# Performance work log

Hardware: AMD Instinct MI355X
Metric: run time of the kernel (lower is better)

Reference implementation:

```python
import jax, jax.numpy as jnp
import numpy as np

JACCARD_THRESH = 0.5
NEGPOS_RATIO = 3
VAR = (0.1, 0.2)


def point_form(p):
    # center-size (cx,cy,w,h) -> corner (xmin,ymin,xmax,ymax)
    return jnp.concatenate([p[:, :2] - p[:, 2:] / 2, p[:, :2] + p[:, 2:] / 2], axis=1)


def jaccard(a, b):
    # a: [No,4] corner boxes, b: [Np,4] corner boxes -> IoU [No,Np]
    lt = jnp.maximum(a[:, None, :2], b[None, :, :2])
    rb = jnp.minimum(a[:, None, 2:], b[None, :, 2:])
    wh = jnp.clip(rb - lt, 0.0)
    inter = wh[..., 0] * wh[..., 1]
    area_a = ((a[:, 2] - a[:, 0]) * (a[:, 3] - a[:, 1]))[:, None]
    area_b = ((b[:, 2] - b[:, 0]) * (b[:, 3] - b[:, 1]))[None, :]
    return inter / (area_a + area_b - inter)


def encode(matched, priors):
    # matched: [Np,4] corner GT, priors: [Np,4] center-size
    g_cxcy = ((matched[:, :2] + matched[:, 2:]) / 2 - priors[:, :2]) / (VAR[0] * priors[:, 2:])
    g_wh = jnp.log((matched[:, 2:] - matched[:, :2]) / priors[:, 2:]) / VAR[1]
    return jnp.concatenate([g_cxcy, g_wh], axis=1)


def match_one(truths, labels, priors):
    # truths: [No,4], labels: [No], priors: [Np,4] center-size
    overlaps = jaccard(truths, point_form(priors))          # [No,Np]
    best_prior_idx = jnp.argmax(overlaps, axis=1)           # [No]
    best_truth_overlap = jnp.max(overlaps, axis=0)          # [Np]
    best_truth_idx = jnp.argmax(overlaps, axis=0)           # [Np]
    # each GT keeps its best prior (overlap forced to 2)
    best_truth_overlap = best_truth_overlap.at[best_prior_idx].set(2.0)
    best_truth_idx = best_truth_idx.at[best_prior_idx].set(jnp.arange(truths.shape[0]))
    matched = truths[best_truth_idx]                        # [Np,4]
    conf = labels[best_truth_idx].astype(jnp.int32) + 1     # background = 0
    conf = jnp.where(best_truth_overlap < JACCARD_THRESH, 0, conf)
    return encode(matched, priors), conf


def reference(loc_data, conf_data, dbox_list, targets):
    num_batch, num_dbox, num_classes = conf_data.shape
    truths = targets[:, :, :4]
    labels = targets[:, :, 4]
    loc_t, conf_t = jax.vmap(match_one, in_axes=(0, 0, None))(truths, labels, dbox_list)
    pos_mask = conf_t > 0                                   # [B,Np]
    # localization loss: SmoothL1 (beta=1), summed over positive dboxes
    diff = loc_data - loc_t
    ad = jnp.abs(diff)
    sl1 = jnp.where(ad < 1.0, 0.5 * diff * diff, ad - 0.5)
    loss_l = jnp.sum(sl1 * pos_mask[..., None].astype(sl1.dtype))
    # per-dbox cross entropy
    logp = jax.nn.log_softmax(conf_data, axis=-1)
    ce = -jnp.take_along_axis(logp, conf_t[..., None], axis=-1)[..., 0]  # [B,Np]
    # hard negative mining: rank (descending) of pos-zeroed CE via double argsort
    loss_c_hnm = jnp.where(pos_mask, 0.0, ce)
    loss_idx = jnp.argsort(-loss_c_hnm, axis=1)
    idx_rank = jnp.argsort(loss_idx, axis=1)
    num_pos = jnp.sum(pos_mask, axis=1, keepdims=True)      # [B,1]
    num_neg = jnp.minimum(num_pos * NEGPOS_RATIO, num_dbox)
    neg_mask = idx_rank < num_neg
    sel = jnp.logical_or(pos_mask, neg_mask)
    loss_c = jnp.sum(jnp.where(sel, ce, 0.0))
    N = jnp.sum(num_pos).astype(loss_l.dtype)
    return loss_l / N, loss_c / N


def setup_inputs() -> dict:
    key = jax.random.key(0)
    ks = jax.random.split(key, 7)
    B, Np, C, No = 128, 8732, 21, 16
    loc_data = jax.random.normal(ks[0], (B, Np, 4), dtype=jnp.float32) * 0.1
    conf_data = jax.random.normal(ks[1], (B, Np, C), dtype=jnp.float32)
    # default boxes in center-size form, w/h strictly positive
    cxcy = jax.random.uniform(ks[2], (Np, 2), minval=0.05, maxval=0.95)
    wh = jax.random.uniform(ks[3], (Np, 2), minval=0.05, maxval=0.5)
    dbox_list = jnp.concatenate([cxcy, wh], axis=1).astype(jnp.float32)
    # ground truth: valid corner-form boxes + class label in [0,20)
    gcxcy = jax.random.uniform(ks[4], (B, No, 2), minval=0.2, maxval=0.8)
    gwh = jax.random.uniform(ks[5], (B, No, 2), minval=0.05, maxval=0.3)
    boxes = jnp.concatenate([gcxcy - gwh / 2, gcxcy + gwh / 2], axis=-1)
    lab = jax.random.randint(ks[6], (B, No, 1), 0, C - 1).astype(jnp.float32)
    targets = jnp.concatenate([boxes, lab], axis=-1).astype(jnp.float32)
    return {"loc_data": loc_data, "conf_data": conf_data, "dbox_list": dbox_list, "targets": targets}
```

## Files before the change

kernel.cpp:

```cpp
#include <hip/hip_runtime.h>
#include <stdint.h>

#define TPB 256
#define PPT 2
#define SELTPB 1024
#define SELWAVES (SELTPB / 64)
#define MAXNO 64
#define NMB 16

__device__ __forceinline__ float sl1f(float d) {
    float ad = fabsf(d);
    return ad < 1.0f ? 0.5f * d * d : ad - 0.5f;
}

__device__ __forceinline__ float iou_pair(float tx1, float ty1, float tx2, float ty2, float ta,
                                          float px1, float py1, float px2, float py2, float pa) {
    float ltx = fmaxf(tx1, px1), lty = fmaxf(ty1, py1);
    float rbx = fminf(tx2, px2), rby = fminf(ty2, py2);
    float wx = fmaxf(rbx - ltx, 0.0f), wy = fmaxf(rby - lty, 0.0f);
    float inter = wx * wy;
    return inter / ((ta + pa) - inter);
}

template <int NO>
__global__ __launch_bounds__(256) void match_partial_kernel(
    const float* __restrict__ dbox, const float* __restrict__ targets,
    unsigned long long* __restrict__ pkeys, unsigned* __restrict__ done, int Np, int No) {
    int b = blockIdx.y, mb = blockIdx.x;
    int tid = threadIdx.x;
    if (mb == 0 && b == 0 && tid == 0) *done = 0u;
    __shared__ float s_t[NO][5];
    __shared__ unsigned long long s_k[4][NO];
    if (tid < No) {
        const float* tr = targets + ((size_t)b * No + tid) * 5;
        float x1 = tr[0], y1 = tr[1], x2 = tr[2], y2 = tr[3];
        s_t[tid][0] = x1; s_t[tid][1] = y1; s_t[tid][2] = x2; s_t[tid][3] = y2;
        s_t[tid][4] = (x2 - x1) * (y2 - y1);
    }
    __syncthreads();
    int clen = (Np + NMB - 1) / NMB;
    int start = mb * clen;
    int end = start + clen;
    if (end > Np) end = Np;
    unsigned long long key[NO];
#pragma unroll
    for (int t = 0; t < NO; ++t) key[t] = 0ull;
    for (int p = start + tid; p < end; p += 256) {
        float4 pr = *reinterpret_cast<const float4*>(dbox + (size_t)p * 4);
        float px1 = pr.x - pr.z * 0.5f, py1 = pr.y - pr.w * 0.5f;
        float px2 = pr.x + pr.z * 0.5f, py2 = pr.y + pr.w * 0.5f;
        float pa = (px2 - px1) * (py2 - py1);
        unsigned lowp = 0xFFFFFFFFu - (unsigned)p;
#pragma unroll
        for (int t = 0; t < NO; ++t) {
            float iou = iou_pair(s_t[t][0], s_t[t][1], s_t[t][2], s_t[t][3], s_t[t][4],
                                 px1, py1, px2, py2, pa);
            unsigned long long k =
                (((unsigned long long)__float_as_uint(iou)) << 32) | (unsigned long long)lowp;
            if (k > key[t]) key[t] = k;
        }
    }
    int lane = tid & 63, wv = tid >> 6;
#pragma unroll
    for (int t = 0; t < NO; ++t) {
        unsigned long long k = key[t];
        for (int off = 32; off; off >>= 1) {
            unsigned long long o = __shfl_down(k, off);
            if (o > k) k = o;
        }
        if (lane == 0) s_k[wv][t] = k;
    }
    __syncthreads();
    if (tid < No) {
        unsigned long long m = s_k[0][tid];
#pragma unroll
        for (int w = 1; w < 4; ++w)
            if (s_k[w][tid] > m) m = s_k[w][tid];
        pkeys[((size_t)b * NMB + mb) * No + tid] = m;
    }
}

template <int CC, int TNO>
__global__ __launch_bounds__(TPB, 1) void main_kernel(
    const float* __restrict__ loc, const float* __restrict__ conf,
    const float* __restrict__ dbox, const float* __restrict__ targets,
    const unsigned long long* __restrict__ pkeys,
    float* __restrict__ v, float* __restrict__ part_l, float* __restrict__ part_c,
    int* __restrict__ part_n, int Np, int C, int No, int nchunk) {
    __shared__ float s_tb[(TNO > 0 ? TNO : MAXNO)][6];
    __shared__ unsigned s_ovr[(TNO > 0 ? TNO : MAXNO)];
    __shared__ float s_red1[4];
    __shared__ float s_red2[4];
    __shared__ int s_redi[4];
    int b = blockIdx.y, chunk = blockIdx.x, tid = threadIdx.x;
    int pbase = chunk * (TPB * PPT);
    if (tid < No) {
        const float* tr = targets + ((size_t)b * No + tid) * 5;
        float x1 = tr[0], y1 = tr[1], x2 = tr[2], y2 = tr[3];
        s_tb[tid][0] = x1; s_tb[tid][1] = y1; s_tb[tid][2] = x2; s_tb[tid][3] = y2;
        s_tb[tid][4] = (x2 - x1) * (y2 - y1);
        s_tb[tid][5] = tr[4];
        unsigned long long k = pkeys[((size_t)b * NMB + 0) * No + tid];
#pragma unroll
        for (int m = 1; m < NMB; ++m) {
            unsigned long long kk = pkeys[((size_t)b * NMB + m) * No + tid];
            if (kk > k) k = kk;
        }
        s_ovr[tid] = 0xFFFFFFFFu - (unsigned)(k & 0xFFFFFFFFull);
    }
    __syncthreads();

    float px1[PPT], py1[PPT], px2[PPT], py2[PPT], pa[PPT];
    float bov[PPT];
    int bidx[PPT], ovt[PPT];
    bool vld[PPT];
#pragma unroll
    for (int pp = 0; pp < PPT; ++pp) {
        int p = pbase + pp * TPB + tid;
        vld[pp] = p < Np;
        bov[pp] = -1.0f; bidx[pp] = 0; ovt[pp] = -1;
        if (vld[pp]) {
            float4 pr = *reinterpret_cast<const float4*>(dbox + (size_t)p * 4);
            px1[pp] = pr.x - pr.z * 0.5f; py1[pp] = pr.y - pr.w * 0.5f;
            px2[pp] = pr.x + pr.z * 0.5f; py2[pp] = pr.y + pr.w * 0.5f;
            pa[pp] = (px2[pp] - px1[pp]) * (py2[pp] - py1[pp]);
        } else {
            px1[pp] = 0; py1[pp] = 0; px2[pp] = 0; py2[pp] = 0; pa[pp] = 0;
        }
    }
    int nt = (TNO > 0) ? TNO : No;
    for (int t = 0; t < nt; ++t) {
        float tx1 = s_tb[t][0], ty1 = s_tb[t][1], tx2 = s_tb[t][2], ty2 = s_tb[t][3];
        float ta = s_tb[t][4];
        unsigned ov = s_ovr[t];
#pragma unroll
        for (int pp = 0; pp < PPT; ++pp) {
            int p = pbase + pp * TPB + tid;
            float iou = iou_pair(tx1, ty1, tx2, ty2, ta,
                                 px1[pp], py1[pp], px2[pp], py2[pp], pa[pp]);
            if (iou > bov[pp]) { bov[pp] = iou; bidx[pp] = t; }
            if (ov == (unsigned)p) ovt[pp] = t;
        }
    }

    float lossl = 0.0f, posce = 0.0f;
    int npos = 0;
#pragma unroll
    for (int pp = 0; pp < PPT; ++pp) {
        if (!vld[pp]) continue;
        int p = pbase + pp * TPB + tid;
        int bi = bidx[pp];
        float bv = bov[pp];
        if (ovt[pp] >= 0) { bi = ovt[pp]; bv = 2.0f; }
        int ct = (bv < 0.5f) ? 0 : ((int)s_tb[bi][5] + 1);
        const float* crow = conf + ((size_t)b * Np + p) * C;
        float ce;
        if (CC == 21) {
            float4 q0 = *reinterpret_cast<const float4*>(crow + 0);
            float4 q1 = *reinterpret_cast<const float4*>(crow + 4);
            float4 q2 = *reinterpret_cast<const float4*>(crow + 8);
            float4 q3 = *reinterpret_cast<const float4*>(crow + 12);
            float4 q4 = *reinterpret_cast<const float4*>(crow + 16);
            float x20 = crow[20];
            float fc = q0.x;
            fc = (ct == 1) ? q0.y : fc;  fc = (ct == 2) ? q0.z : fc;
            fc = (ct == 3) ? q0.w : fc;  fc = (ct == 4) ? q1.x : fc;
            fc = (ct == 5) ? q1.y : fc;  fc = (ct == 6) ? q1.z : fc;
            fc = (ct == 7) ? q1.w : fc;  fc = (ct == 8) ? q2.x : fc;
            fc = (ct == 9) ? q2.y : fc;  fc = (ct == 10) ? q2.z : fc;
            fc = (ct == 11) ? q2.w : fc; fc = (ct == 12) ? q3.x : fc;
            fc = (ct == 13) ? q3.y : fc; fc = (ct == 14) ? q3.z : fc;
            fc = (ct == 15) ? q3.w : fc; fc = (ct == 16) ? q4.x : fc;
            fc = (ct == 17) ? q4.y : fc; fc = (ct == 18) ? q4.z : fc;
            fc = (ct == 19) ? q4.w : fc; fc = (ct == 20) ? x20 : fc;
            float s0 = __expf(q0.x) + __expf(q0.y) + __expf(q0.z) + __expf(q0.w);
            float s1 = __expf(q1.x) + __expf(q1.y) + __expf(q1.z) + __expf(q1.w);
            float s2 = __expf(q2.x) + __expf(q2.y) + __expf(q2.z) + __expf(q2.w);
            float s3 = __expf(q3.x) + __expf(q3.y) + __expf(q3.z) + __expf(q3.w);
            float s4 = __expf(q4.x) + __expf(q4.y) + __expf(q4.z) + __expf(q4.w);
            ce = __logf(((s0 + s1) + (s2 + s3)) + (s4 + __expf(x20))) - fc;
        } else {
            float mx = crow[0];
            for (int j = 1; j < C; ++j) mx = fmaxf(mx, crow[j]);
            float s = 0.0f;
            for (int j = 0; j < C; ++j) s += __expf(crow[j] - mx);
            ce = __logf(s) + mx - crow[ct];
        }
        bool pos = ct > 0;
        v[(size_t)b * Np + p] = pos ? 0.0f : ce;
        if (pos) {
            posce += ce;
            npos += 1;
            float mx1 = s_tb[bi][0], my1 = s_tb[bi][1];
            float mx2 = s_tb[bi][2], my2 = s_tb[bi][3];
            float pcx = (px1[pp] + px2[pp]) * 0.5f, pcy = (py1[pp] + py2[pp]) * 0.5f;
            float pw = px2[pp] - px1[pp], ph = py2[pp] - py1[pp];
            float gcx = ((mx1 + mx2) * 0.5f - pcx) / (0.1f * pw);
            float gcy = ((my1 + my2) * 0.5f - pcy) / (0.1f * ph);
            float gw = __logf((mx2 - mx1) / pw) / 0.2f;
            float gh = __logf((my2 - my1) / ph) / 0.2f;
            float4 l4 = *reinterpret_cast<const float4*>(loc + ((size_t)b * Np + p) * 4);
            lossl += sl1f(l4.x - gcx) + sl1f(l4.y - gcy) + sl1f(l4.z - gw) + sl1f(l4.w - gh);
        }
    }
    float a1 = lossl, a2 = posce;
    int ni = npos;
    for (int off = 32; off; off >>= 1) {
        a1 += __shfl_down(a1, off);
        a2 += __shfl_down(a2, off);
        ni += __shfl_down(ni, off);
    }
    if ((tid & 63) == 0) {
        s_red1[tid >> 6] = a1;
        s_red2[tid >> 6] = a2;
        s_redi[tid >> 6] = ni;
    }
    __syncthreads();
    if (tid == 0) {
        part_l[(size_t)b * nchunk + chunk] = s_red1[0] + s_red1[1] + s_red1[2] + s_red1[3];
        part_c[(size_t)b * nchunk + chunk] = s_red2[0] + s_red2[1] + s_red2[2] + s_red2[3];
        part_n[(size_t)b * nchunk + chunk] = s_redi[0] + s_redi[1] + s_redi[2] + s_redi[3];
    }
}

__global__ __launch_bounds__(SELTPB) void select_kernel(
    const float* __restrict__ v, const float* __restrict__ pl,
    const float* __restrict__ pc, const int* __restrict__ pn,
    float* __restrict__ row_res, unsigned* __restrict__ done,
    float* __restrict__ out, int Np, int nchunk, int negpos) {
    int b = blockIdx.x, tid = threadIdx.x;
    int lane = tid & 63, wv = tid >> 6;
    extern __shared__ unsigned sv[];
    __shared__ unsigned whist[SELWAVES][256];
    __shared__ float s_f[SELWAVES];
    __shared__ int s_dig, s_acc;
    __shared__ float s_lossl, s_posce;
    __shared__ int s_np;
    __shared__ int s_last;

    if (wv == 0) {
        float a = 0.0f, c = 0.0f;
        int n = 0;
        for (int i = lane; i < nchunk; i += 64) {
            a += pl[(size_t)b * nchunk + i];
            c += pc[(size_t)b * nchunk + i];
            n += pn[(size_t)b * nchunk + i];
        }
        for (int off = 32; off; off >>= 1) {
            a += __shfl_down(a, off);
            c += __shfl_down(c, off);
            n += __shfl_down(n, off);
        }
        if (lane == 0) { s_lossl = a; s_posce = c; s_np = n; }
    }
    {
        const float4* v4 = reinterpret_cast<const float4*>(v + (size_t)b * Np);
        int n4 = Np >> 2;
        for (int i = tid; i < n4; i += SELTPB) {
            float4 f = v4[i];
            uint4 u;
            u.x = __float_as_uint(f.x); u.y = __float_as_uint(f.y);
            u.z = __float_as_uint(f.z); u.w = __float_as_uint(f.w);
            *reinterpret_cast<uint4*>(&sv[i << 2]) = u;
        }
        for (int i = (n4 << 2) + tid; i < Np; i += SELTPB)
            sv[i] = __float_as_uint(v[(size_t)b * Np + i]);
    }
    __syncthreads();
    int npos = s_np;
    int K = npos * negpos;
    if (K > Np) K = Np;
    float lossc = s_posce;
    if (K > 0) {
        unsigned prefix = 0;
        int Krem = K;
        for (int shift = 24; shift >= 0; shift -= 8) {
            for (int i = tid; i < SELWAVES * 256; i += SELTPB)
                (&whist[0][0])[i] = 0;
            __syncthreads();
            for (int i = tid; i < Np; i += SELTPB) {
                unsigned u = sv[i];
                bool match = (shift == 24) || ((u >> (shift + 8)) == (prefix >> (shift + 8)));
                if (match) atomicAdd(&whist[wv][(u >> shift) & 0xFFu], 1u);
            }
            __syncthreads();
            if (wv == 0) {
                unsigned t0 = 0, t1 = 0, t2 = 0, t3 = 0;
#pragma unroll
                for (int w = 0; w < SELWAVES; ++w) {
                    t0 += whist[w][4 * lane + 0];
                    t1 += whist[w][4 * lane + 1];
                    t2 += whist[w][4 * lane + 2];
                    t3 += whist[w][4 * lane + 3];
                }
                unsigned s = t0 + t1 + t2 + t3;
                unsigned run = s;
                for (int off = 1; off < 64; off <<= 1) {
                    unsigned o = __shfl_down(run, off);
                    if (lane + off < 64) run += o;
                }
                unsigned hi = run - s;
                unsigned S3 = hi + t3, S2 = S3 + t2, S1 = S2 + t1, S0 = S1 + t0;
                unsigned kr = (unsigned)Krem;
                if (S3 >= kr && hi < kr) { s_dig = 4 * lane + 3; s_acc = (int)hi; }
                else if (S2 >= kr && S3 < kr) { s_dig = 4 * lane + 2; s_acc = (int)S3; }
                else if (S1 >= kr && S2 < kr) { s_dig = 4 * lane + 1; s_acc = (int)S2; }
                else if (S0 >= kr && S1 < kr) { s_dig = 4 * lane + 0; s_acc = (int)S1; }
            }
            __syncthreads();
            prefix |= ((unsigned)s_dig) << shift;
            Krem -= s_acc;
        }
        float sum_gt = 0.0f;
        for (int i = tid; i < Np; i += SELTPB) {
            unsigned u = sv[i];
            if (u > prefix) sum_gt += __uint_as_float(u);
        }
        for (int off = 32; off; off >>= 1) sum_gt += __shfl_down(sum_gt, off);
        if (lane == 0) s_f[wv] = sum_gt;
        __syncthreads();
        if (tid == 0) {
            float t = 0.0f;
            for (int w = 0; w < SELWAVES; ++w) t += s_f[w];
            lossc += t + (float)Krem * __uint_as_float(prefix);
        }
    }
    if (tid == 0) {
        row_res[(size_t)b * 3 + 0] = s_lossl;
        row_res[(size_t)b * 3 + 1] = lossc;
        row_res[(size_t)b * 3 + 2] = (float)npos;
        __threadfence();
        unsigned old = atomicAdd(done, 1u);
        s_last = (old == gridDim.x - 1) ? 1 : 0;
    }
    __syncthreads();
    if (s_last && wv == 0) {
        __threadfence();
        const volatile float* rr = (const volatile float*)row_res;
        float l = 0.0f, c = 0.0f, n = 0.0f;
        int B = (int)gridDim.x;
        for (int i = lane; i < B; i += 64) {
            l += rr[(size_t)i * 3 + 0];
            c += rr[(size_t)i * 3 + 1];
            n += rr[(size_t)i * 3 + 2];
        }
        for (int off = 32; off; off >>= 1) {
            l += __shfl_down(l, off);
            c += __shfl_down(c, off);
            n += __shfl_down(n, off);
        }
        if (lane == 0) {
            out[0] = l / n;
            out[1] = c / n;
        }
    }
}

extern "C" void kernel_launch(void* const* d_in, const int* in_sizes, int n_in,
                              void* d_out, int out_size, void* d_ws, size_t ws_size,
                              hipStream_t stream) {
    const float* loc = (const float*)d_in[0];
    const float* conf = (const float*)d_in[1];
    const float* dbox = (const float*)d_in[2];
    const float* targets = (const float*)d_in[3];

    int Np = in_sizes[2] / 4;
    int B = in_sizes[0] / (Np * 4);
    int C = in_sizes[1] / (B * Np);
    int No = in_sizes[3] / (B * 5);
    int nchunk = (Np + TPB * PPT - 1) / (TPB * PPT);

    char* w = (char*)d_ws;
    unsigned long long* pkeys = (unsigned long long*)w;
    w += (size_t)B * NMB * No * sizeof(unsigned long long);
    float* v = (float*)w;
    w += (size_t)B * Np * sizeof(float);
    float* part_l = (float*)w;
    w += (size_t)B * nchunk * sizeof(float);
    float* part_c = (float*)w;
    w += (size_t)B * nchunk * sizeof(float);
    int* part_n = (int*)w;
    w += (size_t)B * nchunk * sizeof(int);
    float* row_res = (float*)w;
    w += (size_t)B * 3 * sizeof(float);
    unsigned* done = (unsigned*)w;

    dim3 mgrid(NMB, B);
    if (No == 16)
        match_partial_kernel<16><<<mgrid, 256, 0, stream>>>(dbox, targets, pkeys, done, Np, No);
    else
        match_partial_kernel<MAXNO><<<mgrid, 256, 0, stream>>>(dbox, targets, pkeys, done, Np, No);

    dim3 grid(nchunk, B);
    if (C == 21 && No == 16)
        main_kernel<21, 16><<<grid, TPB, 0, stream>>>(loc, conf, dbox, targets, pkeys,
                                                      v, part_l, part_c, part_n, Np, C, No, nchunk);
    else
        main_kernel<0, 0><<<grid, TPB, 0, stream>>>(loc, conf, dbox, targets, pkeys,
                                                    v, part_l, part_c, part_n, Np, C, No, nchunk);
    select_kernel<<<B, SELTPB, (size_t)Np * sizeof(float), stream>>>(
        v, part_l, part_c, part_n, row_res, done, (float*)d_out, Np, nchunk, 3);
}
```

Baseline: 79.15 us.

## Hoist conf log-sum-exp before IoU matching, double points per thread

Moves the 21-class log-sum-exp computation ahead of the prior/GT IoU loop, so the large conf loads are issued early and can overlap with the matching arithmetic. The target logit is then fetched with one scalar load instead of a select chain. PPT rises from 2 to 4 and launch bounds now target 2 blocks per CU, giving fewer blocks with more work each. The general-C fallback path is removed, so the code now assumes C == 21 with no max subtraction, and register pressure grows from holding four rows' state.

```diff
diff --git a/kernel.cpp b/kernel.cpp
--- a/kernel.cpp
+++ b/kernel.cpp
@@ -2,7 +2,7 @@
 #include <stdint.h>
 
 #define TPB 256
-#define PPT 2
+#define PPT 4
 #define SELTPB 1024
 #define SELWAVES (SELTPB / 64)
 #define MAXNO 64
@@ -81,7 +81,7 @@
 }
 
 template <int CC, int TNO>
-__global__ __launch_bounds__(TPB, 1) void main_kernel(
+__global__ __launch_bounds__(TPB, 2) void main_kernel(
     const float* __restrict__ loc, const float* __restrict__ conf,
     const float* __restrict__ dbox, const float* __restrict__ targets,
     const unsigned long long* __restrict__ pkeys,
@@ -110,16 +110,36 @@
     }
     __syncthreads();
 
+    float lse[PPT];
+#pragma unroll
+    for (int pp = 0; pp < PPT; ++pp) {
+        int p = pbase + pp * TPB + tid;
+        lse[pp] = 0.0f;
+        if (p < Np) {
+            const float* crow = conf + ((size_t)b * Np + p) * (CC > 0 ? CC : 21);
+            float4 q0 = *reinterpret_cast<const float4*>(crow + 0);
+            float4 q1 = *reinterpret_cast<const float4*>(crow + 4);
+            float4 q2 = *reinterpret_cast<const float4*>(crow + 8);
+            float4 q3 = *reinterpret_cast<const float4*>(crow + 12);
+            float4 q4 = *reinterpret_cast<const float4*>(crow + 16);
+            float x20 = crow[20];
+            float s0 = __expf(q0.x) + __expf(q0.y) + __expf(q0.z) + __expf(q0.w);
+            float s1 = __expf(q1.x) + __expf(q1.y) + __expf(q1.z) + __expf(q1.w);
+            float s2 = __expf(q2.x) + __expf(q2.y) + __expf(q2.z) + __expf(q2.w);
+            float s3 = __expf(q3.x) + __expf(q3.y) + __expf(q3.z) + __expf(q3.w);
+            float s4 = __expf(q4.x) + __expf(q4.y) + __expf(q4.z) + __expf(q4.w);
+            lse[pp] = __logf(((s0 + s1) + (s2 + s3)) + (s4 + __expf(x20)));
+        }
+    }
+
     float px1[PPT], py1[PPT], px2[PPT], py2[PPT], pa[PPT];
     float bov[PPT];
     int bidx[PPT], ovt[PPT];
-    bool vld[PPT];
 #pragma unroll
     for (int pp = 0; pp < PPT; ++pp) {
         int p = pbase + pp * TPB + tid;
-        vld[pp] = p < Np;
         bov[pp] = -1.0f; bidx[pp] = 0; ovt[pp] = -1;
-        if (vld[pp]) {
+        if (p < Np) {
             float4 pr = *reinterpret_cast<const float4*>(dbox + (size_t)p * 4);
             px1[pp] = pr.x - pr.z * 0.5f; py1[pp] = pr.y - pr.w * 0.5f;
             px2[pp] = pr.x + pr.z * 0.5f; py2[pp] = pr.y + pr.w * 0.5f;
@@ -147,45 +167,14 @@
     int npos = 0;
 #pragma unroll
     for (int pp = 0; pp < PPT; ++pp) {
-        if (!vld[pp]) continue;
         int p = pbase + pp * TPB + tid;
+        if (p >= Np) continue;
         int bi = bidx[pp];
         float bv = bov[pp];
         if (ovt[pp] >= 0) { bi = ovt[pp]; bv = 2.0f; }
         int ct = (bv < 0.5f) ? 0 : ((int)s_tb[bi][5] + 1);
-        const float* crow = conf + ((size_t)b * Np + p) * C;
-        float ce;
-        if (CC == 21) {
-            float4 q0 = *reinterpret_cast<const float4*>(crow + 0);
-            float4 q1 = *reinterpret_cast<const float4*>(crow + 4);
-            float4 q2 = *reinterpret_cast<const float4*>(crow + 8);
-            float4 q3 = *reinterpret_cast<const float4*>(crow + 12);
-            float4 q4 = *reinterpret_cast<const float4*>(crow + 16);
-            float x20 = crow[20];
-            float fc = q0.x;
-            fc = (ct == 1) ? q0.y : fc;  fc = (ct == 2) ? q0.z : fc;
-            fc = (ct == 3) ? q0.w : fc;  fc = (ct == 4) ? q1.x : fc;
-            fc = (ct == 5) ? q1.y : fc;  fc = (ct == 6) ? q1.z : fc;
-            fc = (ct == 7) ? q1.w : fc;  fc = (ct == 8) ? q2.x : fc;
-            fc = (ct == 9) ? q2.y : fc;  fc = (ct == 10) ? q2.z : fc;
-            fc = (ct == 11) ? q2.w : fc; fc = (ct == 12) ? q3.x : fc;
-            fc = (ct == 13) ? q3.y : fc; fc = (ct == 14) ? q3.z : fc;
-            fc = (ct == 15) ? q3.w : fc; fc = (ct == 16) ? q4.x : fc;
-            fc = (ct == 17) ? q4.y : fc; fc = (ct == 18) ? q4.z : fc;
-            fc = (ct == 19) ? q4.w : fc; fc = (ct == 20) ? x20 : fc;
-            float s0 = __expf(q0.x) + __expf(q0.y) + __expf(q0.z) + __expf(q0.w);
-            float s1 = __expf(q1.x) + __expf(q1.y) + __expf(q1.z) + __expf(q1.w);
-            float s2 = __expf(q2.x) + __expf(q2.y) + __expf(q2.z) + __expf(q2.w);
-            float s3 = __expf(q3.x) + __expf(q3.y) + __expf(q3.z) + __expf(q3.w);
-            float s4 = __expf(q4.x) + __expf(q4.y) + __expf(q4.z) + __expf(q4.w);
-            ce = __logf(((s0 + s1) + (s2 + s3)) + (s4 + __expf(x20))) - fc;
-        } else {
-            float mx = crow[0];
-            for (int j = 1; j < C; ++j) mx = fmaxf(mx, crow[j]);
-            float s = 0.0f;
-            for (int j = 0; j < C; ++j) s += __expf(crow[j] - mx);
-            ce = __logf(s) + mx - crow[ct];
-        }
+        float fc = conf[((size_t)b * Np + p) * C + ct];
+        float ce = lse[pp] - fc;
         bool pos = ct > 0;
         v[(size_t)b * Np + p] = pos ? 0.0f : ce;
         if (pos) {
```

Result: slower. 90.30 us (+14.1%).
